# Performance work log

Hardware: AMD Instinct MI355X
Metric: run time of the kernel (lower is better)

The kernel has to match this reference:

```python
import jax, jax.numpy as jnp
import numpy as np

D, H, O, E, K = 512, 2048, 512, 8, 2
CF = 1.0  # capacity_factor


def setup_inputs() -> dict:
    key = jax.random.key(0)
    ks = jax.random.split(key, 4)
    s = lambda k, shape, sc: jax.random.normal(k, shape, jnp.float32) * sc
    return {
        "x": s(ks[0], (8, 2048, D), 1.0),
        "gate_w": s(ks[1], (D, E), D ** -0.5),
        "gate_b": jnp.zeros((E,), jnp.float32),
        "w1": s(ks[2], (E, D, H), D ** -0.5),
        "b1": jnp.zeros((E, H), jnp.float32),
        "w2": s(ks[3], (E, H, O), H ** -0.5),
        "b2": jnp.zeros((E, O), jnp.float32),
    }


def _moe(x, gate_w, gate_b, w1, b1, w2, b2):
    orig = x.shape
    xf = x.reshape(-1, orig[-1])            # [N, D]
    N = xf.shape[0]
    capacity = max(int((N / E) * CF), 4)    # static (shape-derived)

    logits = xf @ gate_w + gate_b           # [N, E]
    gate_probs = jax.nn.softmax(logits, axis=-1)
    topk_p, topk_i = jax.lax.top_k(gate_probs, K)          # [N, K]
    norm_p = topk_p / topk_p.sum(-1, keepdims=True)        # [N, K]

    hot = jax.nn.one_hot(topk_i, E, dtype=xf.dtype)        # [N, K, E]
    mask = hot.sum(1)                                      # [N, E] in {0,1} (top-k indices unique)
    w_te = (norm_p[..., None] * hot).sum(1)                # [N, E] routing weight per token/expert

    def dispatch(m):
        # m: [N] 0/1 mask for one expert; keep first `capacity` tokens in token order
        cs = jnp.cumsum(m)
        keep = (m > 0) & (cs <= capacity)
        idx = jnp.argsort(jnp.where(keep, 0, 1), stable=True)[:capacity]  # kept tokens first, in order
        valid = jnp.arange(capacity) < keep.sum()
        return idx, valid

    idx, valid = jax.vmap(dispatch)(mask.T)                # idx: [E, cap], valid: [E, cap]

    gathered = xf[idx]                                     # [E, cap, D]
    h = jax.nn.gelu(jnp.einsum('ecd,edh->ech', gathered, w1) + b1[:, None, :], approximate=False)
    out = jnp.einsum('ech,eho->eco', h, w2) + b2[:, None, :]  # [E, cap, O]

    wg = w_te[idx, jnp.arange(E)[:, None]]                 # [E, cap] gate weight per dispatched token
    contrib = out * (wg * valid.astype(out.dtype))[..., None]
    combined = jnp.zeros((N, O), out.dtype).at[idx.reshape(-1)].add(contrib.reshape(-1, O))
    return combined.reshape(*orig[:-1], O), gate_probs


def reference(x, gate_w, gate_b, w1, b1, w2, b2):
    return _moe(x, gate_w, gate_b, w1, b1, w2, b2)
```

## Files before the change

kernel.cpp:

```cpp
#include <hip/hip_runtime.h>
#include <hip/hip_bf16.h>

#define NTOK 16384
#define DDIM 512
#define HDIM 2048
#define ODIM 512
#define NE 8
#define CAP 2048

typedef __attribute__((ext_vector_type(8))) short short8v;
typedef __attribute__((ext_vector_type(4))) short short4v;
typedef __attribute__((ext_vector_type(8))) unsigned short ushort8v;
typedef __attribute__((ext_vector_type(4))) float f32x4;

static __device__ __forceinline__ unsigned short f2bf(float f) {
  __hip_bfloat16 h = __float2bfloat16(f);
  return __builtin_bit_cast(unsigned short, h);
}
static __device__ __forceinline__ float bf2f(unsigned short u) {
  unsigned int x = ((unsigned int)u) << 16;
  return __builtin_bit_cast(float, x);
}

#define GLOAD_LDS16(gp, lp)                                               \
  __builtin_amdgcn_global_load_lds(                                       \
      (const __attribute__((address_space(1))) void*)(gp),                \
      (__attribute__((address_space(3))) void*)(lp), 16, 0, 0)

__device__ __forceinline__ void transpose_block(const float* __restrict__ src,
                                                __hip_bfloat16* __restrict__ dst,
                                                int R, int C, int b) {
  __shared__ float tile[32][33];
  int nx = C >> 5, ny = R >> 5;
  int x = b % nx, y = (b / nx) % ny, e = b / (nx * ny);
  size_t base = (size_t)e * R * C;
  int c0 = x * 32, r0 = y * 32;
  int tx = threadIdx.x & 31, ty = threadIdx.x >> 5;
#pragma unroll
  for (int i = 0; i < 32; i += 8)
    tile[ty + i][tx] = src[base + (size_t)(r0 + ty + i) * C + c0 + tx];
  __syncthreads();
#pragma unroll
  for (int i = 0; i < 32; i += 8)
    dst[base + (size_t)(c0 + ty + i) * R + r0 + tx] = __float2bfloat16(tile[tx][ty + i]);
}

__global__ void k_prep(const float* __restrict__ x, const float* __restrict__ gw,
                       const float* __restrict__ gb, const float* __restrict__ w1,
                       __hip_bfloat16* __restrict__ w1t, const float* __restrict__ w2,
                       __hip_bfloat16* __restrict__ w2t, float* __restrict__ gate_probs,
                       int2* __restrict__ tk_e, float2* __restrict__ tk_w,
                       int* __restrict__ token_slot) {
  int b = blockIdx.x;
  if (b < 8192) { transpose_block(w1, w1t, DDIM, HDIM, b); return; }
  if (b < 16384) { transpose_block(w2, w2t, HDIM, ODIM, b - 8192); return; }
  b -= 16384;
  __shared__ float gws[DDIM * 9];
  int tid = threadIdx.x;
  for (int i = tid; i < DDIM * NE; i += 256) {
    int d = i >> 3, e = i & 7;
    gws[d * 9 + e] = gw[i];
  }
  __syncthreads();
  int wid = tid >> 6, lane = tid & 63;
  int t = b * 4 + wid;
  const float* xr = x + (size_t)t * DDIM;
  float acc[NE] = {0.f, 0.f, 0.f, 0.f, 0.f, 0.f, 0.f, 0.f};
#pragma unroll
  for (int j = 0; j < 8; ++j) {
    float xv = xr[lane + 64 * j];
    const float* g = &gws[(lane + 64 * j) * 9];
#pragma unroll
    for (int e = 0; e < NE; ++e) acc[e] += xv * g[e];
  }
#pragma unroll
  for (int e = 0; e < NE; ++e) {
#pragma unroll
    for (int off = 32; off > 0; off >>= 1) acc[e] += __shfl_xor(acc[e], off, 64);
  }
  if (lane == 0) {
    float p[NE];
    float m = -1e30f;
#pragma unroll
    for (int e = 0; e < NE; ++e) { p[e] = acc[e] + gb[e]; m = fmaxf(m, p[e]); }
    float s = 0.f;
#pragma unroll
    for (int e = 0; e < NE; ++e) { p[e] = expf(p[e] - m); s += p[e]; }
    float inv = 1.f / s;
#pragma unroll
    for (int e = 0; e < NE; ++e) { p[e] *= inv; gate_probs[(size_t)t * NE + e] = p[e]; }
    int i1 = 0; float p1 = p[0];
#pragma unroll
    for (int e = 1; e < NE; ++e) if (p[e] > p1) { p1 = p[e]; i1 = e; }
    int i2 = -1; float p2 = -1e30f;
#pragma unroll
    for (int e = 0; e < NE; ++e) if (e != i1 && p[e] > p2) { p2 = p[e]; i2 = e; }
    float wsum = p1 + p2;
    tk_e[t] = make_int2(i1, i2);
    tk_w[t] = make_float2(p1 / wsum, p2 / wsum);
    token_slot[2 * t] = -1;
    token_slot[2 * t + 1] = -1;
  }
}

__global__ void k_dispatch(const int2* __restrict__ tk_e, int* __restrict__ token_slot,
                           int* __restrict__ expert_tokens) {
  int e = blockIdx.x;
  int tid = threadIdx.x;
  int lane = tid & 63, w = tid >> 6;
  __shared__ int wave_cnt[16];
  int base = 0;
  for (int chunk = 0; chunk < NTOK / 1024; ++chunk) {
    int t = chunk * 1024 + tid;
    int2 te = tk_e[t];
    int k = (te.x == e) ? 0 : ((te.y == e) ? 1 : -1);
    bool flag = (k >= 0);
    unsigned long long m = __ballot(flag);
    int pre = __popcll(m & ((1ull << lane) - 1ull));
    __syncthreads();
    if (lane == 0) wave_cnt[w] = __popcll(m);
    __syncthreads();
    int off = 0, total = 0;
#pragma unroll
    for (int i = 0; i < 16; ++i) {
      off += (i < w) ? wave_cnt[i] : 0;
      total += wave_cnt[i];
    }
    int rank = base + off + pre;
    if (flag && rank < CAP) {
      expert_tokens[e * CAP + rank] = t;
      token_slot[2 * t + k] = e * CAP + rank;
    }
    base += total;
  }
  int nvalid = base < CAP ? base : CAP;
  for (int s = nvalid + tid; s < CAP; s += 1024)
    expert_tokens[e * CAP + s] = 0;
}

__global__ void k_gather(const float* __restrict__ x,
                         const int* __restrict__ expert_tokens,
                         __hip_bfloat16* __restrict__ xg) {
  int tid = threadIdx.x, wid = tid >> 6, lane = tid & 63;
  int slot = blockIdx.x * 4 + wid;
  int tok = expert_tokens[slot];
  const float4* src = reinterpret_cast<const float4*>(x + (size_t)tok * DDIM) + lane * 2;
  float4 u = src[0], v = src[1];
  ushort8v o;
  o[0] = f2bf(u.x); o[1] = f2bf(u.y); o[2] = f2bf(u.z); o[3] = f2bf(u.w);
  o[4] = f2bf(v.x); o[5] = f2bf(v.y); o[6] = f2bf(v.z); o[7] = f2bf(v.w);
  *reinterpret_cast<ushort8v*>(xg + (size_t)slot * DDIM + lane * 8) = o;
}

static __device__ __forceinline__ float gelu_fast(float v) {
  float z = 1.5957691216057308f * (v + 0.044715f * v * v * v);
  return v / (1.f + __expf(-z));
}

template <int K, int M, bool GELU, typename OutT>
__global__ __launch_bounds__(256, 3) void k_gemm(
    const __hip_bfloat16* __restrict__ A, const __hip_bfloat16* __restrict__ B,
    const float* __restrict__ bias, OutT* __restrict__ C) {
  __shared__ char lds[3][16384];
  int gx = gridDim.x, gy = gridDim.y;
  int lin = (blockIdx.z * gy + blockIdx.y) * gx + blockIdx.x;
  int total = gx * gy * (int)gridDim.z;
  int cpx = total >> 3;
  lin = (lin & 7) * cpx + (lin >> 3);
  int gxy = gx * gy;
  int e = lin / gxy;
  int rem = lin - e * gxy;
  int mt = rem / gx, nt = rem - mt * gx;

  const int m0 = mt * 128, n0 = nt * 128;
  const int tid = threadIdx.x;
  const int lane = tid & 63, wid = tid >> 6;
  const int wr = wid >> 1, wc = wid & 1;
  const int lrow = lane & 15, kseg = lane >> 4;

  const int r0 = tid >> 2;
  const int sc = (tid & 3) ^ ((r0 >> 1) & 3);
  const int cb0 = (tid & 192) * 16;
  const int cb1 = 4096 + cb0;
  const __hip_bfloat16* Ab = A + ((size_t)e * M + m0) * K;
  const __hip_bfloat16* Bb = B + ((size_t)e * CAP + n0) * K;

#define STAGE(buf, kk)                                                         \
  do {                                                                         \
    GLOAD_LDS16(Ab + (size_t)r0 * K + (kk) + sc * 8, lds[buf] + cb0);          \
    GLOAD_LDS16(Ab + (size_t)(r0 + 64) * K + (kk) + sc * 8, lds[buf] + cb1);   \
    GLOAD_LDS16(Bb + (size_t)r0 * K + (kk) + sc * 8, lds[buf] + 8192 + cb0);   \
    GLOAD_LDS16(Bb + (size_t)(r0 + 64) * K + (kk) + sc * 8, lds[buf] + 8192 + cb1); \
  } while (0)

#define READF(fa, fb, bi)                                                      \
  do {                                                                         \
    const char* AsB_ = lds[bi];                                                \
    const char* BsB_ = lds[bi] + 8192;                                         \
    _Pragma("unroll")                                                          \
    for (int mm = 0; mm < 4; ++mm) {                                           \
      int rr = wr * 64 + mm * 16 + lrow;                                       \
      int ks = kseg ^ ((rr >> 1) & 3);                                         \
      fa[mm] = *reinterpret_cast<const short8v*>(AsB_ + rr * 64 + ks * 16);    \
    }                                                                          \
    _Pragma("unroll")                                                          \
    for (int nn = 0; nn < 4; ++nn) {                                           \
      int rr = wc * 64 + nn * 16 + lrow;                                       \
      int ks = kseg ^ ((rr >> 1) & 3);                                         \
      fb[nn] = *reinterpret_cast<const short8v*>(BsB_ + rr * 64 + ks * 16);    \
    }                                                                          \
  } while (0)

#define MFMA16(fa, fb)                                                         \
  do {                                                                         \
    __builtin_amdgcn_s_setprio(1);                                             \
    _Pragma("unroll")                                                          \
    for (int mm = 0; mm < 4; ++mm)                                             \
      _Pragma("unroll")                                                        \
      for (int nn = 0; nn < 4; ++nn)                                           \
        acc[mm][nn] = __builtin_amdgcn_mfma_f32_16x16x32_bf16(                 \
            fa[mm], fb[nn], acc[mm][nn], 0, 0, 0);                             \
    __builtin_amdgcn_s_setprio(0);                                             \
  } while (0)

#define LGKM0_FENCE()                                                          \
  do {                                                                         \
    asm volatile("s_waitcnt lgkmcnt(0)" ::: "memory");                         \
    __builtin_amdgcn_sched_barrier(0);                                         \
  } while (0)

  f32x4 acc[4][4] = {};
  short8v pa[4], pb[4], qa[4], qb[4];
  const int T = K >> 5;

  STAGE(0, 0);
  STAGE(1, 32);
  STAGE(2, 64);
  asm volatile("s_waitcnt vmcnt(8)" ::: "memory");
  __builtin_amdgcn_s_barrier();
  READF(pa, pb, 0);
  LGKM0_FENCE();

  int bt = 0;
  for (int t = 0; t < T; t += 2) {
    int b1 = (bt == 2) ? 0 : bt + 1;
    int b2 = (b1 == 2) ? 0 : b1 + 1;
    if (t + 2 < T) asm volatile("s_waitcnt vmcnt(4)" ::: "memory");
    else           asm volatile("s_waitcnt vmcnt(0)" ::: "memory");
    __builtin_amdgcn_s_barrier();
    READF(qa, qb, b1);
    if (t + 3 < T) STAGE(bt, (t + 3) * 32);
    __builtin_amdgcn_sched_barrier(0);
    MFMA16(pa, pb);
    LGKM0_FENCE();
    if (t + 2 < T) {
      if (t + 3 < T) asm volatile("s_waitcnt vmcnt(4)" ::: "memory");
      else           asm volatile("s_waitcnt vmcnt(0)" ::: "memory");
      __builtin_amdgcn_s_barrier();
      READF(pa, pb, b2);
      if (t + 4 < T) STAGE(b1, (t + 4) * 32);
      __builtin_amdgcn_sched_barrier(0);
    }
    MFMA16(qa, qb);
    LGKM0_FENCE();
    bt = b2;
  }
#undef STAGE
#undef READF
#undef MFMA16
#undef LGKM0_FENCE

#pragma unroll
  for (int mm = 0; mm < 4; ++mm) {
    int mrow = m0 + wr * 64 + mm * 16 + kseg * 4;
    float4 bv = *reinterpret_cast<const float4*>(&bias[e * M + mrow]);
#pragma unroll
    for (int nn = 0; nn < 4; ++nn) {
      int token = n0 + wc * 64 + nn * 16 + lrow;
      float v0 = acc[mm][nn][0] + bv.x;
      float v1 = acc[mm][nn][1] + bv.y;
      float v2 = acc[mm][nn][2] + bv.z;
      float v3 = acc[mm][nn][3] + bv.w;
      if (GELU) {
        v0 = gelu_fast(v0); v1 = gelu_fast(v1);
        v2 = gelu_fast(v2); v3 = gelu_fast(v3);
      }
      OutT* cp = C + ((size_t)e * CAP + token) * M + mrow;
      if constexpr (__is_same(OutT, __hip_bfloat16)) {
        short4v o;
        o[0] = (short)f2bf(v0); o[1] = (short)f2bf(v1);
        o[2] = (short)f2bf(v2); o[3] = (short)f2bf(v3);
        *reinterpret_cast<short4v*>(cp) = o;
      } else {
        float4 o = {v0, v1, v2, v3};
        *reinterpret_cast<float4*>(cp) = o;
      }
    }
  }
}

__global__ void k_combine(const __hip_bfloat16* __restrict__ outbuf,
                          const int* __restrict__ token_slot,
                          const float2* __restrict__ tk_w,
                          float* __restrict__ comb) {
  int tid = threadIdx.x;
  int wid = tid >> 6, lane = tid & 63;
  int t = blockIdx.x * 4 + wid;
  int s0 = token_slot[2 * t], s1 = token_slot[2 * t + 1];
  float2 w = tk_w[t];
  float r[8] = {0.f, 0.f, 0.f, 0.f, 0.f, 0.f, 0.f, 0.f};
  if (s0 >= 0) {
    ushort8v a = *reinterpret_cast<const ushort8v*>(outbuf + (size_t)s0 * ODIM + lane * 8);
#pragma unroll
    for (int j = 0; j < 8; ++j) r[j] += w.x * bf2f(a[j]);
  }
  if (s1 >= 0) {
    ushort8v a = *reinterpret_cast<const ushort8v*>(outbuf + (size_t)s1 * ODIM + lane * 8);
#pragma unroll
    for (int j = 0; j < 8; ++j) r[j] += w.y * bf2f(a[j]);
  }
  float4* q = reinterpret_cast<float4*>(comb + (size_t)t * ODIM + lane * 8);
  float4 o0 = {r[0], r[1], r[2], r[3]};
  float4 o1 = {r[4], r[5], r[6], r[7]};
  q[0] = o0;
  q[1] = o1;
}

extern "C" void kernel_launch(void* const* d_in, const int* in_sizes, int n_in,
                              void* d_out, int out_size, void* d_ws, size_t ws_size,
                              hipStream_t stream) {
  const float* x      = (const float*)d_in[0];
  const float* gate_w = (const float*)d_in[1];
  const float* gate_b = (const float*)d_in[2];
  const float* w1     = (const float*)d_in[3];
  const float* b1     = (const float*)d_in[4];
  const float* w2     = (const float*)d_in[5];
  const float* b2     = (const float*)d_in[6];

  float* comb = (float*)d_out;
  float* gate_probs = comb + (size_t)NTOK * ODIM;

  char* ws = (char*)d_ws;
  __hip_bfloat16* w1t    = (__hip_bfloat16*)(ws);
  __hip_bfloat16* w2t    = (__hip_bfloat16*)(ws + 16777216);
  __hip_bfloat16* hbuf   = (__hip_bfloat16*)(ws + 33554432);
  __hip_bfloat16* xg     = (__hip_bfloat16*)(ws + 100663296);
  __hip_bfloat16* outbuf = (__hip_bfloat16*)(ws + 117440512);
  int*   expert_tokens   = (int*)(ws + 134217728);
  int2*  tk_e            = (int2*)(ws + 134283264);
  float2* tk_w           = (float2*)(ws + 134414336);
  int*   token_slot      = (int*)(ws + 134545408);

  k_prep<<<16384 + NTOK / 4, 256, 0, stream>>>(x, gate_w, gate_b, w1, w1t, w2, w2t,
                                               gate_probs, tk_e, tk_w, token_slot);
  k_dispatch<<<NE, 1024, 0, stream>>>(tk_e, token_slot, expert_tokens);
  k_gather<<<NE * CAP / 4, 256, 0, stream>>>(x, expert_tokens, xg);
  k_gemm<DDIM, HDIM, true, __hip_bfloat16>
      <<<dim3(CAP / 128, HDIM / 128, NE), 256, 0, stream>>>(w1t, xg, b1, hbuf);
  k_gemm<HDIM, ODIM, false, __hip_bfloat16>
      <<<dim3(CAP / 128, ODIM / 128, NE), 256, 0, stream>>>(w2t, hbuf, b2, outbuf);
  k_combine<<<NTOK / 4, 256, 0, stream>>>(outbuf, token_slot, tk_w, comb);
}
```

Baseline: 167.8 us.

## Fuse token gather into first expert GEMM via indirect row loads

The gate kernel now also writes a bf16 copy of x, and the first GEMM loads its token rows straight from that copy through the expert_tokens index list. This removes the separate gather kernel and the staging buffer it filled. The GEMM main loop is also fully unrolled with compile-time buffer indices, and its per-row pointers are precomputed. The bf16 copy of x covers all tokens rather than only the dispatched slots, and the indirect B rows lose the contiguity the gathered layout had.

```diff
diff --git a/kernel.cpp b/kernel.cpp
--- a/kernel.cpp
+++ b/kernel.cpp
@@ -50,7 +50,7 @@
                        __hip_bfloat16* __restrict__ w1t, const float* __restrict__ w2,
                        __hip_bfloat16* __restrict__ w2t, float* __restrict__ gate_probs,
                        int2* __restrict__ tk_e, float2* __restrict__ tk_w,
-                       int* __restrict__ token_slot) {
+                       int* __restrict__ token_slot, __hip_bfloat16* __restrict__ xbf) {
   int b = blockIdx.x;
   if (b < 8192) { transpose_block(w1, w1t, DDIM, HDIM, b); return; }
   if (b < 16384) { transpose_block(w2, w2t, HDIM, ODIM, b - 8192); return; }
@@ -66,13 +66,17 @@
   int t = b * 4 + wid;
   const float* xr = x + (size_t)t * DDIM;
   float acc[NE] = {0.f, 0.f, 0.f, 0.f, 0.f, 0.f, 0.f, 0.f};
+  float xv[8];
 #pragma unroll
   for (int j = 0; j < 8; ++j) {
-    float xv = xr[lane + 64 * j];
+    xv[j] = xr[lane + 64 * j];
     const float* g = &gws[(lane + 64 * j) * 9];
 #pragma unroll
-    for (int e = 0; e < NE; ++e) acc[e] += xv * g[e];
-  }
+    for (int e = 0; e < NE; ++e) acc[e] += xv[j] * g[e];
+  }
+  __hip_bfloat16* xb = xbf + (size_t)t * DDIM + lane;
+#pragma unroll
+  for (int j = 0; j < 8; ++j) xb[64 * j] = __float2bfloat16(xv[j]);
 #pragma unroll
   for (int e = 0; e < NE; ++e) {
 #pragma unroll
@@ -138,29 +142,16 @@
     expert_tokens[e * CAP + s] = 0;
 }
 
-__global__ void k_gather(const float* __restrict__ x,
-                         const int* __restrict__ expert_tokens,
-                         __hip_bfloat16* __restrict__ xg) {
-  int tid = threadIdx.x, wid = tid >> 6, lane = tid & 63;
-  int slot = blockIdx.x * 4 + wid;
-  int tok = expert_tokens[slot];
-  const float4* src = reinterpret_cast<const float4*>(x + (size_t)tok * DDIM) + lane * 2;
-  float4 u = src[0], v = src[1];
-  ushort8v o;
-  o[0] = f2bf(u.x); o[1] = f2bf(u.y); o[2] = f2bf(u.z); o[3] = f2bf(u.w);
-  o[4] = f2bf(v.x); o[5] = f2bf(v.y); o[6] = f2bf(v.z); o[7] = f2bf(v.w);
-  *reinterpret_cast<ushort8v*>(xg + (size_t)slot * DDIM + lane * 8) = o;
-}
-
 static __device__ __forceinline__ float gelu_fast(float v) {
   float z = 1.5957691216057308f * (v + 0.044715f * v * v * v);
   return v / (1.f + __expf(-z));
 }
 
-template <int K, int M, bool GELU, typename OutT>
+template <int K, int M, bool GELU, bool INDIR, typename OutT>
 __global__ __launch_bounds__(256, 3) void k_gemm(
     const __hip_bfloat16* __restrict__ A, const __hip_bfloat16* __restrict__ B,
-    const float* __restrict__ bias, OutT* __restrict__ C) {
+    const float* __restrict__ bias, OutT* __restrict__ C,
+    const int* __restrict__ etok) {
   __shared__ char lds[3][16384];
   int gx = gridDim.x, gy = gridDim.y;
   int lin = (blockIdx.z * gy + blockIdx.y) * gx + blockIdx.x;
@@ -182,15 +173,26 @@
   const int sc = (tid & 3) ^ ((r0 >> 1) & 3);
   const int cb0 = (tid & 192) * 16;
   const int cb1 = 4096 + cb0;
-  const __hip_bfloat16* Ab = A + ((size_t)e * M + m0) * K;
-  const __hip_bfloat16* Bb = B + ((size_t)e * CAP + n0) * K;
+  const __hip_bfloat16* Ap0 = A + ((size_t)e * M + m0 + r0) * K + sc * 8;
+  const __hip_bfloat16* Ap1 = Ap0 + (size_t)64 * K;
+  const __hip_bfloat16* Bp0;
+  const __hip_bfloat16* Bp1;
+  if constexpr (INDIR) {
+    int t0 = etok[e * CAP + n0 + r0];
+    int t1 = etok[e * CAP + n0 + r0 + 64];
+    Bp0 = B + (size_t)t0 * K + sc * 8;
+    Bp1 = B + (size_t)t1 * K + sc * 8;
+  } else {
+    Bp0 = B + ((size_t)e * CAP + n0 + r0) * K + sc * 8;
+    Bp1 = Bp0 + (size_t)64 * K;
+  }
 
 #define STAGE(buf, kk)                                                         \
   do {                                                                         \
-    GLOAD_LDS16(Ab + (size_t)r0 * K + (kk) + sc * 8, lds[buf] + cb0);          \
-    GLOAD_LDS16(Ab + (size_t)(r0 + 64) * K + (kk) + sc * 8, lds[buf] + cb1);   \
-    GLOAD_LDS16(Bb + (size_t)r0 * K + (kk) + sc * 8, lds[buf] + 8192 + cb0);   \
-    GLOAD_LDS16(Bb + (size_t)(r0 + 64) * K + (kk) + sc * 8, lds[buf] + 8192 + cb1); \
+    GLOAD_LDS16(Ap0 + (kk), lds[buf] + cb0);                                   \
+    GLOAD_LDS16(Ap1 + (kk), lds[buf] + cb1);                                   \
+    GLOAD_LDS16(Bp0 + (kk), lds[buf] + 8192 + cb0);                            \
+    GLOAD_LDS16(Bp1 + (kk), lds[buf] + 8192 + cb1);                            \
   } while (0)
 
 #define READF(fa, fb, bi)                                                      \
@@ -231,7 +233,7 @@
 
   f32x4 acc[4][4] = {};
   short8v pa[4], pb[4], qa[4], qb[4];
-  const int T = K >> 5;
+  constexpr int T = K >> 5;
 
   STAGE(0, 0);
   STAGE(1, 32);
@@ -241,10 +243,11 @@
   READF(pa, pb, 0);
   LGKM0_FENCE();
 
-  int bt = 0;
+#pragma unroll
   for (int t = 0; t < T; t += 2) {
-    int b1 = (bt == 2) ? 0 : bt + 1;
-    int b2 = (b1 == 2) ? 0 : b1 + 1;
+    const int bt = t % 3;
+    const int b1 = (t + 1) % 3;
+    const int b2 = (t + 2) % 3;
     if (t + 2 < T) asm volatile("s_waitcnt vmcnt(4)" ::: "memory");
     else           asm volatile("s_waitcnt vmcnt(0)" ::: "memory");
     __builtin_amdgcn_s_barrier();
@@ -263,7 +266,6 @@
     }
     MFMA16(qa, qb);
     LGKM0_FENCE();
-    bt = b2;
   }
 #undef STAGE
 #undef READF
@@ -344,7 +346,7 @@
   __hip_bfloat16* w1t    = (__hip_bfloat16*)(ws);
   __hip_bfloat16* w2t    = (__hip_bfloat16*)(ws + 16777216);
   __hip_bfloat16* hbuf   = (__hip_bfloat16*)(ws + 33554432);
-  __hip_bfloat16* xg     = (__hip_bfloat16*)(ws + 100663296);
+  __hip_bfloat16* xbf    = (__hip_bfloat16*)(ws + 100663296);
   __hip_bfloat16* outbuf = (__hip_bfloat16*)(ws + 117440512);
   int*   expert_tokens   = (int*)(ws + 134217728);
   int2*  tk_e            = (int2*)(ws + 134283264);
@@ -352,12 +354,13 @@
   int*   token_slot      = (int*)(ws + 134545408);
 
   k_prep<<<16384 + NTOK / 4, 256, 0, stream>>>(x, gate_w, gate_b, w1, w1t, w2, w2t,
-                                               gate_probs, tk_e, tk_w, token_slot);
+                                               gate_probs, tk_e, tk_w, token_slot, xbf);
   k_dispatch<<<NE, 1024, 0, stream>>>(tk_e, token_slot, expert_tokens);
-  k_gather<<<NE * CAP / 4, 256, 0, stream>>>(x, expert_tokens, xg);
-  k_gemm<DDIM, HDIM, true, __hip_bfloat16>
-      <<<dim3(CAP / 128, HDIM / 128, NE), 256, 0, stream>>>(w1t, xg, b1, hbuf);
-  k_gemm<HDIM, ODIM, false, __hip_bfloat16>
-      <<<dim3(CAP / 128, ODIM / 128, NE), 256, 0, stream>>>(w2t, hbuf, b2, outbuf);
+  k_gemm<DDIM, HDIM, true, true, __hip_bfloat16>
+      <<<dim3(CAP / 128, HDIM / 128, NE), 256, 0, stream>>>(
+          w1t, xbf, b1, hbuf, expert_tokens);
+  k_gemm<HDIM, ODIM, false, false, __hip_bfloat16>
+      <<<dim3(CAP / 128, ODIM / 128, NE), 256, 0, stream>>>(
+          w2t, hbuf, b2, outbuf, nullptr);
   k_combine<<<NTOK / 4, 256, 0, stream>>>(outbuf, token_slot, tk_w, comb);
 }
```

Measured after the change: 160.1 us (median of 3 runs). 4.6% less time.
